# Performance work log

Measured on AMD Instinct MI355X. Metric: run time of the kernel, lower is better.

Reference implementation:

```python
import jax, jax.numpy as jnp
import numpy as np

N, E, G, D, L = 100000, 1600000, 64, 128, 4
CLS_HID, NUM_CLASSES = 256, 10
BN_EPS = 1e-5


def setup_inputs() -> dict:
    key = jax.random.key(0)
    ks = jax.random.split(key, 16)
    s = 0.05
    cls_in = D + L * D  # sum(dims) = 640
    return {
        "node_deg": jax.random.randint(ks[0], (N,), 0, D),
        "edge_index": jax.random.randint(ks[1], (2, E), 0, N),
        "batch_vec": jnp.sort(jax.random.randint(ks[2], (N,), 0, G)),
        "eps": jnp.zeros((L,), jnp.float32),  # GINConv train_eps init 0
        "W1": jax.random.normal(ks[3], (L, D, D), jnp.float32) * s,
        "b1": jax.random.normal(ks[4], (L, D), jnp.float32) * s,
        "W2": jax.random.normal(ks[5], (L, D, D), jnp.float32) * s,
        "b2": jax.random.normal(ks[6], (L, D), jnp.float32) * s,
        "bn_g": jnp.ones((L, D), jnp.float32),
        "bn_b": jnp.zeros((L, D), jnp.float32),
        "Wc1": jax.random.normal(ks[7], (cls_in, CLS_HID), jnp.float32) * s,
        "bc1": jax.random.normal(ks[8], (CLS_HID,), jnp.float32) * s,
        "Wc2": jax.random.normal(ks[9], (CLS_HID, NUM_CLASSES), jnp.float32) * s,
        "bc2": jax.random.normal(ks[10], (NUM_CLASSES,), jnp.float32) * s,
    }


def reference(node_deg, edge_index, batch_vec, eps, W1, b1, W2, b2, bn_g, bn_b, Wc1, bc1, Wc2, bc2):
    n = node_deg.shape[0]
    src, dst = edge_index[0], edge_index[1]
    # OneHotEmbedding of node degree -> initial node features [N, D]
    x = jax.nn.one_hot(node_deg, D, dtype=jnp.float32)
    zs = [x]
    for l in range(eps.shape[0]):
        h_in = zs[-1]
        # GINConv: (1+eps)*x + scatter-add of neighbor features
        agg = jax.ops.segment_sum(h_in[src], dst, num_segments=n)
        h = (1.0 + eps[l]) * h_in + agg
        # mlp: lin -> lrelu -> lin
        h = jax.nn.leaky_relu(h @ W1[l] + b1[l])
        h = h @ W2[l] + b2[l]
        # BatchNorm1d over nodes (training-mode batch stats, biased var)
        mean = h.mean(axis=0)
        var = h.var(axis=0)
        h = (h - mean) * jax.lax.rsqrt(var + BN_EPS) * bn_g[l] + bn_b[l]
        zs.append(jax.nn.leaky_relu(h))
    z = jnp.concatenate(zs, axis=1)  # [N, 640]
    pooled = jax.ops.segment_sum(z, batch_vec, num_segments=G)  # global_add_pool
    pooled = jax.nn.leaky_relu(pooled)
    # classifier head: Linear -> LeakyReLU -> Linear (drop_out=0)
    h = jax.nn.leaky_relu(pooled @ Wc1 + bc1)
    return h @ Wc2 + bc2
```

## Files before the change

kernel.cpp:

```cpp
#include <hip/hip_runtime.h>
#include <hip/hip_bf16.h>


#define N_NODES   100000
#define N_EDGES   1600000
#define N_GRAPHS  64
#define DIM       128
#define N_LAYERS  4
#define CLS_IN    640
#define CLS_HID   256
#define N_CLASSES 10
#define LRELU_SLOPE 0.01f
#define BN_EPS_F    1e-5f

#define NBUCK    782
#define BUCK_CAP 4096
#define ECAP2    1024

typedef __attribute__((ext_vector_type(8))) short bf16x8;
typedef __attribute__((ext_vector_type(4))) float f32x4;

__device__ __forceinline__ float lrelu(float x) { return x > 0.f ? x : LRELU_SLOPE * x; }

__device__ __forceinline__ ushort bf16r(float x) {
    uint a = __float_as_uint(x);
    return (ushort)((a + 0x7FFFu + ((a >> 16) & 1u)) >> 16);
}
__device__ __forceinline__ uint pack2(float x, float y) {
    uint a = __float_as_uint(x), b = __float_as_uint(y);
    a = (a + 0x7FFFu + ((a >> 16) & 1u)) >> 16;
    b = (b + 0x7FFFu + ((b >> 16) & 1u)) >> 16;
    return a | (b << 16);
}
__device__ __forceinline__ float2 unpack2(uint v) {
    return make_float2(__uint_as_float(v << 16), __uint_as_float(v & 0xFFFF0000u));
}

__global__ void k_convert_w(const float* __restrict__ W1, const float* __restrict__ W2,
                            ushort* __restrict__ W1t, ushort* __restrict__ W2t,
                            uint* __restrict__ cursor, float* __restrict__ statsA,
                            float* __restrict__ pooled) {
    int gid = blockIdx.x * blockDim.x + threadIdx.x;
    if (blockIdx.x == 0) {
        for (int i = threadIdx.x; i < NBUCK; i += 256) cursor[i] = 0u;
        for (int i = threadIdx.x; i < 4 * 2 * DIM; i += 256) statsA[i] = 0.f;
    }
    for (int i = gid; i < N_GRAPHS * CLS_IN; i += 512 * 256) pooled[i] = 0.f;
    if (gid >= 8 * DIM * DIM) return;
    int mat = gid >> 14, idx = gid & 16383;
    int k = idx >> 7, n = idx & 127;
    const float* src = (mat < 4) ? (W1 + mat * DIM * DIM) : (W2 + (mat - 4) * DIM * DIM);
    ushort* dst = (mat < 4) ? (W1t + mat * DIM * DIM) : (W2t + (mat - 4) * DIM * DIM);
    dst[n * DIM + k] = bf16r(src[k * DIM + n]);
}

__global__ void k_build_x(const int* __restrict__ deg, const int* __restrict__ batch,
                          uint* __restrict__ x, float* __restrict__ pooled) {
    int gid = blockIdx.x * blockDim.x + threadIdx.x;
    if (gid >= N_NODES * 64) return;
    int i = gid >> 6, c = gid & 63;
    int d = deg[i];
    uint v = 0;
    if ((d >> 1) == c) v = 0x3F80u << (16 * (d & 1));
    x[gid] = v;
    if (c == 0) atomicAdd(&pooled[batch[i] * CLS_IN + d], 1.0f);
}

__global__ void __launch_bounds__(1024) k_partition(const int* __restrict__ src,
                                                    const int* __restrict__ dst,
                                                    uint* __restrict__ cursor,
                                                    uint* __restrict__ ebuf) {
    __shared__ uint hist[NBUCK];
    __shared__ uint basev[NBUCK];
    int t = threadIdx.x;
    for (int b = t; b < NBUCK; b += 1024) hist[b] = 0;
    __syncthreads();
    int e0 = blockIdx.x * 16384;
    uint msrc[16], mdst[16], mrank[16];
#pragma unroll
    for (int i = 0; i < 16; ++i) {
        int e = e0 + i * 1024 + t;
        if (e < N_EDGES) {
            msrc[i] = (uint)src[e];
            mdst[i] = (uint)dst[e];
            mrank[i] = atomicAdd(&hist[mdst[i] >> 7], 1u);
        } else mdst[i] = 0xFFFFFFFFu;
    }
    __syncthreads();
    for (int b = t; b < NBUCK; b += 1024) {
        uint c = hist[b];
        basev[b] = c ? (uint)(b * BUCK_CAP) + atomicAdd(&cursor[b], c) : 0u;
    }
    __syncthreads();
#pragma unroll
    for (int i = 0; i < 16; ++i) {
        if (mdst[i] != 0xFFFFFFFFu) {
            uint b = mdst[i] >> 7;
            ebuf[basev[b] + mrank[i]] = ((mdst[i] & 127u) << 17) | msrc[i];
        }
    }
}

__global__ void __launch_bounds__(1024) k_bases(const uint* __restrict__ cursor,
                                                uint* __restrict__ base,
                                                int* __restrict__ indptr) {
    __shared__ uint sh[1024];
    int t = threadIdx.x;
    uint v = (t < NBUCK) ? min(cursor[t], (uint)BUCK_CAP) : 0u;
    sh[t] = v; __syncthreads();
    for (int off = 1; off < 1024; off <<= 1) {
        uint add = (t >= off) ? sh[t - off] : 0u;
        __syncthreads();
        sh[t] += add;
        __syncthreads();
    }
    if (t < NBUCK) base[t] = sh[t] - v;
    if (t == NBUCK - 1) indptr[N_NODES] = (int)sh[t];
}

__global__ void __launch_bounds__(512) k_sort(const uint* __restrict__ ebuf,
                                              const uint* __restrict__ cursor,
                                              const uint* __restrict__ base,
                                              int* __restrict__ csr,
                                              int* __restrict__ indptr) {
    __shared__ uint sortedL[BUCK_CAP];
    __shared__ uint hist[128];
    __shared__ uint startv[129];
    const int t = threadIdx.x, b = blockIdx.x;
    int cnt = (int)cursor[b]; if (cnt > BUCK_CAP) cnt = BUCK_CAP;
    if (t < 128) hist[t] = 0;
    __syncthreads();
    uint ent[8], rank[8];
    const uint* ep = ebuf + b * BUCK_CAP;
#pragma unroll
    for (int k = 0; k < 8; ++k) {
        int i = t + k * 512;
        if (i < cnt) { ent[k] = ep[i]; rank[k] = atomicAdd(&hist[ent[k] >> 17], 1u); }
    }
    __syncthreads();
    if (t < 128) startv[t + 1] = hist[t];
    if (t == 0) startv[0] = 0;
    __syncthreads();
    for (int off = 1; off < 128; off <<= 1) {
        uint add = (t < 128 && t >= off) ? startv[t + 1 - off] : 0u;
        __syncthreads();
        if (t < 128 && t >= off) startv[t + 1] += add;
        __syncthreads();
    }
#pragma unroll
    for (int k = 0; k < 8; ++k) {
        int i = t + k * 512;
        if (i < cnt) sortedL[startv[ent[k] >> 17] + rank[k]] = ent[k];
    }
    __syncthreads();
    int gbase = (int)base[b];
    for (int i = t; i < cnt; i += 512)
        csr[gbase + i] = (int)(sortedL[i] & 0x1FFFFu);
    if (t < 128) {
        int node = b * 128 + t;
        if (node < N_NODES) indptr[node] = gbase + (int)startv[t];
    }
}

__global__ void __launch_bounds__(128) k_agg6(const uint* __restrict__ h,
                                              const int* __restrict__ indptr,
                                              const int* __restrict__ csr,
                                              uint* __restrict__ out,
                                              const float* __restrict__ epsv, int layer) {
    __shared__ int eL[ECAP2];
    __shared__ int sv[33];
    const int t = threadIdx.x, lane = t & 63, wave = t >> 6;
    const int half = lane >> 5, c = lane & 31;
    const int node0 = blockIdx.x * 32;
    if (t < 33) {
        int n = node0 + t;
        sv[t] = indptr[n > N_NODES ? N_NODES : n];
    }
    __syncthreads();
    const int gbase = sv[0];
    const int cnt = sv[32] - gbase;
    const bool inLds = (cnt <= ECAP2);
    {
        int stg = inLds ? cnt : 0;
        for (int i = t; i < stg; i += 128) eL[i] = csr[gbase + i];
    }
    __syncthreads();
    const float s = 1.0f + epsv[layer];
    for (int ri = 0; ri < 16; ++ri) {
        int r = wave * 16 + ri;
        int g = node0 + r;
        if (g >= N_NODES) break;
        int beg = sv[r] - gbase, end = sv[r + 1] - gbase;
        float a0, a1, a2, a3;
        {
            uint2 own = half ? make_uint2(0u, 0u)
                             : ((const uint2*)(h + (size_t)g * 64))[c];
            float2 o0 = unpack2(own.x), o1 = unpack2(own.y);
            a0 = s * o0.x; a1 = s * o0.y; a2 = s * o1.x; a3 = s * o1.y;
        }
        int j = beg;
        if (inLds) {
            for (; j + 8 <= end; j += 8) {
                int i0 = eL[j + half],     i1 = eL[j + 2 + half];
                int i2 = eL[j + 4 + half], i3 = eL[j + 6 + half];
                uint2 w0 = ((const uint2*)(h + (size_t)i0 * 64))[c];
                uint2 w1 = ((const uint2*)(h + (size_t)i1 * 64))[c];
                uint2 w2 = ((const uint2*)(h + (size_t)i2 * 64))[c];
                uint2 w3 = ((const uint2*)(h + (size_t)i3 * 64))[c];
                float2 p;
                p = unpack2(w0.x); a0 += p.x; a1 += p.y;
                p = unpack2(w0.y); a2 += p.x; a3 += p.y;
                p = unpack2(w1.x); a0 += p.x; a1 += p.y;
                p = unpack2(w1.y); a2 += p.x; a3 += p.y;
                p = unpack2(w2.x); a0 += p.x; a1 += p.y;
                p = unpack2(w2.y); a2 += p.x; a3 += p.y;
                p = unpack2(w3.x); a0 += p.x; a1 += p.y;
                p = unpack2(w3.y); a2 += p.x; a3 += p.y;
            }
            for (; j < end; j += 2) {
                int jj = j + half;
                bool valid = jj < end;
                int iu = eL[valid ? jj : j];
                uint2 w = ((const uint2*)(h + (size_t)iu * 64))[c];
                if (valid) {
                    float2 p;
                    p = unpack2(w.x); a0 += p.x; a1 += p.y;
                    p = unpack2(w.y); a2 += p.x; a3 += p.y;
                }
            }
        } else {
            for (; j < end; j += 2) {
                int jj = j + half;
                bool valid = jj < end;
                int iu = csr[gbase + (valid ? jj : j)];
                uint2 w = ((const uint2*)(h + (size_t)iu * 64))[c];
                if (valid) {
                    float2 p;
                    p = unpack2(w.x); a0 += p.x; a1 += p.y;
                    p = unpack2(w.y); a2 += p.x; a3 += p.y;
                }
            }
        }
        a0 += __shfl_xor(a0, 32);
        a1 += __shfl_xor(a1, 32);
        a2 += __shfl_xor(a2, 32);
        a3 += __shfl_xor(a3, 32);
        if (!half) {
            uint2 o;
            o.x = pack2(a0, a1);
            o.y = pack2(a2, a3);
            ((uint2*)(out + (size_t)g * 64))[c] = o;
        }
    }
}

#define MLP_LDS_BYTES 69632
__global__ void __launch_bounds__(256) k_mlp(const ushort* __restrict__ A,
                                             const ushort* __restrict__ W1t,
                                             const float* __restrict__ b1,
                                             const ushort* __restrict__ W2t,
                                             const float* __restrict__ b2,
                                             ushort* __restrict__ C,
                                             float* __restrict__ stats) {
    __shared__ char pool[MLP_LDS_BYTES];
    ushort* As = (ushort*)pool;
    ushort* Ws = (ushort*)(pool + 34816);
    float*  Cs = (float*)pool;
    const int t = threadIdx.x;
    const int row0 = blockIdx.x * 128;
    {
        int r = t >> 1, hh = t & 1;
        uint4* l = (uint4*)(As + r * 136 + hh * 64);
        if (row0 + r < N_NODES) {
            const uint4* g = (const uint4*)(A + (size_t)(row0 + r) * DIM + hh * 64);
#pragma unroll
            for (int k = 0; k < 8; ++k) l[k] = g[k];
        } else {
            uint4 z = make_uint4(0, 0, 0, 0);
#pragma unroll
            for (int k = 0; k < 8; ++k) l[k] = z;
        }
        const uint4* gw = (const uint4*)(W1t + r * DIM + hh * 64);
        uint4* lw = (uint4*)(Ws + r * 136 + hh * 64);
#pragma unroll
        for (int k = 0; k < 8; ++k) lw[k] = gw[k];
    }
    __syncthreads();
    const int lane = t & 63, wave = t >> 6;
    const int q = lane >> 4, m = lane & 15;
    const int R = (wave >> 1) * 64, Cb = (wave & 1) * 64;
    {
        f32x4 acc[4][4] = {};
#pragma unroll
        for (int ks = 0; ks < 4; ++ks) {
            bf16x8 a[4], b[4];
#pragma unroll
            for (int i = 0; i < 4; ++i)
                a[i] = *(const bf16x8*)(As + (R + i * 16 + m) * 136 + ks * 32 + q * 8);
#pragma unroll
            for (int j = 0; j < 4; ++j)
                b[j] = *(const bf16x8*)(Ws + (Cb + j * 16 + m) * 136 + ks * 32 + q * 8);
#pragma unroll
            for (int i = 0; i < 4; ++i)
#pragma unroll
                for (int j = 0; j < 4; ++j)
                    acc[i][j] = __builtin_amdgcn_mfma_f32_16x16x32_bf16(a[i], b[j], acc[i][j], 0, 0, 0);
        }
        __syncthreads();
        float bias1[4];
#pragma unroll
        for (int j = 0; j < 4; ++j) bias1[j] = b1[Cb + j * 16 + m];
#pragma unroll
        for (int i = 0; i < 4; ++i)
#pragma unroll
            for (int j = 0; j < 4; ++j)
#pragma unroll
                for (int r = 0; r < 4; ++r)
                    As[(R + i * 16 + q * 4 + r) * 136 + Cb + j * 16 + m] =
                        bf16r(lrelu(acc[i][j][r] + bias1[j]));
        {
            int r = t >> 1, hh = t & 1;
            const uint4* gw = (const uint4*)(W2t + r * DIM + hh * 64);
            uint4* lw = (uint4*)(Ws + r * 136 + hh * 64);
#pragma unroll
            for (int k = 0; k < 8; ++k) lw[k] = gw[k];
        }
    }
    __syncthreads();
    f32x4 acc2[4][4] = {};
#pragma unroll
    for (int ks = 0; ks < 4; ++ks) {
        bf16x8 a[4], b[4];
#pragma unroll
        for (int i = 0; i < 4; ++i)
            a[i] = *(const bf16x8*)(As + (R + i * 16 + m) * 136 + ks * 32 + q * 8);
#pragma unroll
        for (int j = 0; j < 4; ++j)
            b[j] = *(const bf16x8*)(Ws + (Cb + j * 16 + m) * 136 + ks * 32 + q * 8);
#pragma unroll
        for (int i = 0; i < 4; ++i)
#pragma unroll
            for (int j = 0; j < 4; ++j)
                acc2[i][j] = __builtin_amdgcn_mfma_f32_16x16x32_bf16(a[i], b[j], acc2[i][j], 0, 0, 0);
    }
    __syncthreads();
    float bias2[4];
#pragma unroll
    for (int j = 0; j < 4; ++j) bias2[j] = b2[Cb + j * 16 + m];
#pragma unroll
    for (int i = 0; i < 4; ++i)
#pragma unroll
        for (int j = 0; j < 4; ++j)
#pragma unroll
            for (int r = 0; r < 4; ++r)
                Cs[(R + i * 16 + q * 4 + r) * 132 + Cb + j * 16 + m] = acc2[i][j][r] + bias2[j];
    __syncthreads();
    if (t < DIM) {
        int rows = N_NODES - row0; if (rows > 128) rows = 128;
        float s1 = 0.f, s2 = 0.f;
        for (int r = 0; r < rows; ++r) { float v = Cs[r * 132 + t]; s1 += v; s2 += v * v; }
        atomicAdd(&stats[t], s1);
        atomicAdd(&stats[DIM + t], s2);
    }
    {
        int r = t >> 1, hh = t & 1;
        if (row0 + r < N_NODES) {
            uint4* outp = (uint4*)(C + (size_t)(row0 + r) * DIM + hh * 64);
#pragma unroll
            for (int k = 0; k < 8; ++k) {
                float4 v0 = *(const float4*)(Cs + r * 132 + hh * 64 + k * 8);
                float4 v1 = *(const float4*)(Cs + r * 132 + hh * 64 + k * 8 + 4);
                uint4 o;
                o.x = pack2(v0.x, v0.y); o.y = pack2(v0.z, v0.w);
                o.z = pack2(v1.x, v1.y); o.w = pack2(v1.z, v1.w);
                outp[k] = o;
            }
        }
    }
}

#define PROWS 64
__global__ void __launch_bounds__(256) k_bnpool(const uint* __restrict__ src,
                                                uint* __restrict__ dst,
                                                const float* __restrict__ stats,
                                                const float* __restrict__ bn_g,
                                                const float* __restrict__ bn_b, int layer,
                                                const int* __restrict__ batch,
                                                float* __restrict__ pooled, int colOff) {
    int c = threadIdx.x & 63;
    int chunk = threadIdx.x >> 6;
    int r0 = blockIdx.x * PROWS + chunk * (PROWS / 4);
    float sc0, sh0, sc1, sh1;
    {
        int f0 = 2 * c, f1 = 2 * c + 1;
        float m0 = stats[f0] * (1.0f / N_NODES);
        float m1 = stats[f1] * (1.0f / N_NODES);
        float v0 = stats[DIM + f0] * (1.0f / N_NODES) - m0 * m0;
        float v1 = stats[DIM + f1] * (1.0f / N_NODES) - m1 * m1;
        sc0 = bn_g[layer * DIM + f0] * rsqrtf(v0 + BN_EPS_F);
        sc1 = bn_g[layer * DIM + f1] * rsqrtf(v1 + BN_EPS_F);
        sh0 = bn_b[layer * DIM + f0] - m0 * sc0;
        sh1 = bn_b[layer * DIM + f1] - m1 * sc1;
    }
    int curg = -1;
    float a0 = 0.f, a1 = 0.f;
    for (int i = 0; i < PROWS / 4; ++i) {
        int r = r0 + i;
        if (r >= N_NODES) break;
        float2 v = unpack2(src[r * 64 + c]);
        float x0 = lrelu(v.x * sc0 + sh0);
        float x1 = lrelu(v.y * sc1 + sh1);
        dst[r * 64 + c] = pack2(x0, x1);
        int g = batch[r];
        if (g != curg) {
            if (curg >= 0) {
                atomicAdd(&pooled[curg * CLS_IN + colOff + 2 * c], a0);
                atomicAdd(&pooled[curg * CLS_IN + colOff + 2 * c + 1], a1);
            }
            curg = g; a0 = 0.f; a1 = 0.f;
        }
        a0 += x0; a1 += x1;
    }
    if (curg >= 0) {
        atomicAdd(&pooled[curg * CLS_IN + colOff + 2 * c], a0);
        atomicAdd(&pooled[curg * CLS_IN + colOff + 2 * c + 1], a1);
    }
}

__global__ void __launch_bounds__(256) k_classifier(const float* __restrict__ pooled,
                                                    const float* __restrict__ Wc1,
                                                    const float* __restrict__ bc1,
                                                    const float* __restrict__ Wc2,
                                                    const float* __restrict__ bc2,
                                                    float* __restrict__ out) {
    __shared__ float p[CLS_IN];
    __shared__ float hh[CLS_HID];
    int g = blockIdx.x, t = threadIdx.x;
    for (int j = t; j < CLS_IN; j += 256) p[j] = lrelu(pooled[g * CLS_IN + j]);
    __syncthreads();
    float acc = bc1[t];
    for (int k = 0; k < CLS_IN; ++k) acc += p[k] * Wc1[k * CLS_HID + t];
    hh[t] = lrelu(acc);
    __syncthreads();
    if (t < N_CLASSES) {
        float a2 = bc2[t];
        for (int k = 0; k < CLS_HID; ++k) a2 += hh[k] * Wc2[k * N_CLASSES + t];
        out[g * N_CLASSES + t] = a2;
    }
}

extern "C" void kernel_launch(void* const* d_in, const int* in_sizes, int n_in,
                              void* d_out, int out_size, void* d_ws, size_t ws_size,
                              hipStream_t stream) {
    const int*   deg   = (const int*)d_in[0];
    const int*   edges = (const int*)d_in[1];
    const int*   srcv  = edges;
    const int*   dstv  = edges + N_EDGES;
    const int*   batch = (const int*)d_in[2];
    const float* epsv  = (const float*)d_in[3];
    const float* W1    = (const float*)d_in[4];
    const float* b1    = (const float*)d_in[5];
    const float* W2    = (const float*)d_in[6];
    const float* b2    = (const float*)d_in[7];
    const float* bn_g  = (const float*)d_in[8];
    const float* bn_b  = (const float*)d_in[9];
    const float* Wc1   = (const float*)d_in[10];
    const float* bc1   = (const float*)d_in[11];
    const float* Wc2   = (const float*)d_in[12];
    const float* bc2   = (const float*)d_in[13];

    char* ws = (char*)d_ws;
    const size_t BUFB = (size_t)N_NODES * DIM * 2;
    size_t off = 0;
    ushort* buf0   = (ushort*)(ws + off); off += BUFB;
    ushort* buf1   = (ushort*)(ws + off); off += BUFB;
    ushort* W1t    = (ushort*)(ws + off); off += 4 * DIM * DIM * 2;
    ushort* W2t    = (ushort*)(ws + off); off += 4 * DIM * DIM * 2;
    float*  pooled = (float*)(ws + off);  off += N_GRAPHS * CLS_IN * 4;
    float*  statsA = (float*)(ws + off);  off += 4 * 2 * DIM * 4;
    uint*   cursor = (uint*)(ws + off);   off += (NBUCK + 8) * 4;
    uint*   base   = (uint*)(ws + off);   off += (NBUCK + 8) * 4;
    int*    indptr = (int*)(ws + off);    off += (N_NODES + 8) * 4;
    int*    csr    = (int*)(ws + off);    off += (size_t)N_EDGES * 4;
    uint*   ebuf   = (uint*)(ws + off);   off += (size_t)NBUCK * BUCK_CAP * 4;

    k_convert_w<<<512, 256, 0, stream>>>(W1, W2, W1t, W2t, cursor, statsA, pooled);
    k_build_x<<<(N_NODES * 64 + 255) / 256, 256, 0, stream>>>(deg, batch, (uint*)buf0, pooled);
    k_partition<<<(N_EDGES + 16383) / 16384, 1024, 0, stream>>>(srcv, dstv, cursor, ebuf);
    k_bases<<<1, 1024, 0, stream>>>(cursor, base, indptr);
    k_sort<<<NBUCK, 512, 0, stream>>>(ebuf, cursor, base, csr, indptr);

    const int gemm_grid = (N_NODES + 127) / 128;
    const int agg_grid  = (N_NODES + 31) / 32;
    for (int l = 0; l < N_LAYERS; ++l) {
        float* stats = statsA + l * 2 * DIM;
        k_agg6<<<agg_grid, 128, 0, stream>>>((const uint*)buf0, indptr, csr,
                                             (uint*)buf1, epsv, l);
        k_mlp<<<gemm_grid, 256, 0, stream>>>(buf1, W1t + l * DIM * DIM, b1 + l * DIM,
                                             W2t + l * DIM * DIM, b2 + l * DIM,
                                             buf1, stats);
        k_bnpool<<<(N_NODES + PROWS - 1) / PROWS, 256, 0, stream>>>(
            (const uint*)buf1, (uint*)buf0, stats, bn_g, bn_b, l, batch,
            pooled, DIM * (l + 1));
    }

    k_classifier<<<N_GRAPHS, 256, 0, stream>>>(pooled, Wc1, bc1, Wc2, bc2, (float*)d_out);
}
```

Measured before the change: 670.3 us.

## Fuse BatchNorm, LeakyReLU and pooling into the next layer's aggregation

The separate per-layer BN/LeakyReLU/pool pass is removed. The MLP now writes raw pre-BN features, and the next layer's aggregation kernel applies the previous layer's BN scale/shift and LeakyReLU on the fly to both the node's own features and every gathered neighbour. The own-node normalized values are also pooled into the graph sums inside that kernel. Only the last layer keeps a standalone pooling kernel. This is meant to save three full read/write passes over the node features, at the cost of redoing the normalization per gathered edge inside the gather loop.

```diff
diff --git a/kernel.cpp b/kernel.cpp
--- a/kernel.cpp
+++ b/kernel.cpp
@@ -20,7 +20,7 @@
 typedef __attribute__((ext_vector_type(8))) short bf16x8;
 typedef __attribute__((ext_vector_type(4))) float f32x4;
 
-__device__ __forceinline__ float lrelu(float x) { return x > 0.f ? x : LRELU_SLOPE * x; }
+__device__ __forceinline__ float lrelu(float x) { return fmaxf(x, LRELU_SLOPE * x); }
 
 __device__ __forceinline__ ushort bf16r(float x) {
     uint a = __float_as_uint(x);
@@ -162,11 +162,16 @@
     }
 }
 
-__global__ void __launch_bounds__(128) k_agg6(const uint* __restrict__ h,
+__global__ void __launch_bounds__(128) k_agg7(const uint* __restrict__ h,
                                               const int* __restrict__ indptr,
                                               const int* __restrict__ csr,
                                               uint* __restrict__ out,
-                                              const float* __restrict__ epsv, int layer) {
+                                              const float* __restrict__ epsv, int layer,
+                                              const float* __restrict__ stats,
+                                              const float* __restrict__ gamma,
+                                              const float* __restrict__ beta,
+                                              const int* __restrict__ batch,
+                                              float* __restrict__ pooled, int colOff) {
     __shared__ int eL[ECAP2];
     __shared__ int sv[33];
     const int t = threadIdx.x, lane = t & 63, wave = t >> 6;
@@ -176,6 +181,21 @@
         int n = node0 + t;
         sv[t] = indptr[n > N_NODES ? N_NODES : n];
     }
+    float sc0 = 1.f, sc1 = 1.f, sc2 = 1.f, sc3 = 1.f;
+    float sh0 = 0.f, sh1 = 0.f, sh2 = 0.f, sh3 = 0.f;
+    const bool doPool = (stats != nullptr);
+    if (doPool) {
+        int f = 4 * c;
+        float m, var, g;
+        m = stats[f] * (1.0f / N_NODES); var = stats[DIM + f] * (1.0f / N_NODES) - m * m;
+        g = gamma[f] * rsqrtf(var + BN_EPS_F); sc0 = g; sh0 = beta[f] - m * g;
+        m = stats[f+1] * (1.0f / N_NODES); var = stats[DIM + f+1] * (1.0f / N_NODES) - m * m;
+        g = gamma[f+1] * rsqrtf(var + BN_EPS_F); sc1 = g; sh1 = beta[f+1] - m * g;
+        m = stats[f+2] * (1.0f / N_NODES); var = stats[DIM + f+2] * (1.0f / N_NODES) - m * m;
+        g = gamma[f+2] * rsqrtf(var + BN_EPS_F); sc2 = g; sh2 = beta[f+2] - m * g;
+        m = stats[f+3] * (1.0f / N_NODES); var = stats[DIM + f+3] * (1.0f / N_NODES) - m * m;
+        g = gamma[f+3] * rsqrtf(var + BN_EPS_F); sc3 = g; sh3 = beta[f+3] - m * g;
+    }
     __syncthreads();
     const int gbase = sv[0];
     const int cnt = sv[32] - gbase;
@@ -186,17 +206,34 @@
     }
     __syncthreads();
     const float s = 1.0f + epsv[layer];
+    int curg = -1;
+    float p0 = 0.f, p1 = 0.f, p2 = 0.f, p3 = 0.f;
     for (int ri = 0; ri < 16; ++ri) {
         int r = wave * 16 + ri;
         int g = node0 + r;
         if (g >= N_NODES) break;
         int beg = sv[r] - gbase, end = sv[r + 1] - gbase;
-        float a0, a1, a2, a3;
-        {
-            uint2 own = half ? make_uint2(0u, 0u)
-                             : ((const uint2*)(h + (size_t)g * 64))[c];
+        float a0 = 0.f, a1 = 0.f, a2 = 0.f, a3 = 0.f;
+        if (!half) {
+            uint2 own = ((const uint2*)(h + (size_t)g * 64))[c];
             float2 o0 = unpack2(own.x), o1 = unpack2(own.y);
-            a0 = s * o0.x; a1 = s * o0.y; a2 = s * o1.x; a3 = s * o1.y;
+            float b0 = lrelu(fmaf(o0.x, sc0, sh0));
+            float b1 = lrelu(fmaf(o0.y, sc1, sh1));
+            float b2 = lrelu(fmaf(o1.x, sc2, sh2));
+            float b3 = lrelu(fmaf(o1.y, sc3, sh3));
+            if (doPool) {
+                int bg = batch[g];
+                if (bg != curg) {
+                    if (curg >= 0) {
+                        float* pp = &pooled[curg * CLS_IN + colOff + 4 * c];
+                        atomicAdd(pp, p0); atomicAdd(pp + 1, p1);
+                        atomicAdd(pp + 2, p2); atomicAdd(pp + 3, p3);
+                    }
+                    curg = bg; p0 = p1 = p2 = p3 = 0.f;
+                }
+                p0 += b0; p1 += b1; p2 += b2; p3 += b3;
+            }
+            a0 = s * b0; a1 = s * b1; a2 = s * b2; a3 = s * b3;
         }
         int j = beg;
         if (inLds) {
@@ -208,14 +245,14 @@
                 uint2 w2 = ((const uint2*)(h + (size_t)i2 * 64))[c];
                 uint2 w3 = ((const uint2*)(h + (size_t)i3 * 64))[c];
                 float2 p;
-                p = unpack2(w0.x); a0 += p.x; a1 += p.y;
-                p = unpack2(w0.y); a2 += p.x; a3 += p.y;
-                p = unpack2(w1.x); a0 += p.x; a1 += p.y;
-                p = unpack2(w1.y); a2 += p.x; a3 += p.y;
-                p = unpack2(w2.x); a0 += p.x; a1 += p.y;
-                p = unpack2(w2.y); a2 += p.x; a3 += p.y;
-                p = unpack2(w3.x); a0 += p.x; a1 += p.y;
-                p = unpack2(w3.y); a2 += p.x; a3 += p.y;
+                p = unpack2(w0.x); a0 += lrelu(fmaf(p.x, sc0, sh0)); a1 += lrelu(fmaf(p.y, sc1, sh1));
+                p = unpack2(w0.y); a2 += lrelu(fmaf(p.x, sc2, sh2)); a3 += lrelu(fmaf(p.y, sc3, sh3));
+                p = unpack2(w1.x); a0 += lrelu(fmaf(p.x, sc0, sh0)); a1 += lrelu(fmaf(p.y, sc1, sh1));
+                p = unpack2(w1.y); a2 += lrelu(fmaf(p.x, sc2, sh2)); a3 += lrelu(fmaf(p.y, sc3, sh3));
+                p = unpack2(w2.x); a0 += lrelu(fmaf(p.x, sc0, sh0)); a1 += lrelu(fmaf(p.y, sc1, sh1));
+                p = unpack2(w2.y); a2 += lrelu(fmaf(p.x, sc2, sh2)); a3 += lrelu(fmaf(p.y, sc3, sh3));
+                p = unpack2(w3.x); a0 += lrelu(fmaf(p.x, sc0, sh0)); a1 += lrelu(fmaf(p.y, sc1, sh1));
+                p = unpack2(w3.y); a2 += lrelu(fmaf(p.x, sc2, sh2)); a3 += lrelu(fmaf(p.y, sc3, sh3));
             }
             for (; j < end; j += 2) {
                 int jj = j + half;
@@ -224,8 +261,8 @@
                 uint2 w = ((const uint2*)(h + (size_t)iu * 64))[c];
                 if (valid) {
                     float2 p;
-                    p = unpack2(w.x); a0 += p.x; a1 += p.y;
-                    p = unpack2(w.y); a2 += p.x; a3 += p.y;
+                    p = unpack2(w.x); a0 += lrelu(fmaf(p.x, sc0, sh0)); a1 += lrelu(fmaf(p.y, sc1, sh1));
+                    p = unpack2(w.y); a2 += lrelu(fmaf(p.x, sc2, sh2)); a3 += lrelu(fmaf(p.y, sc3, sh3));
                 }
             }
         } else {
@@ -236,8 +273,8 @@
                 uint2 w = ((const uint2*)(h + (size_t)iu * 64))[c];
                 if (valid) {
                     float2 p;
-                    p = unpack2(w.x); a0 += p.x; a1 += p.y;
-                    p = unpack2(w.y); a2 += p.x; a3 += p.y;
+                    p = unpack2(w.x); a0 += lrelu(fmaf(p.x, sc0, sh0)); a1 += lrelu(fmaf(p.y, sc1, sh1));
+                    p = unpack2(w.y); a2 += lrelu(fmaf(p.x, sc2, sh2)); a3 += lrelu(fmaf(p.y, sc3, sh3));
                 }
             }
         }
@@ -251,6 +288,11 @@
             o.y = pack2(a2, a3);
             ((uint2*)(out + (size_t)g * 64))[c] = o;
         }
+    }
+    if (doPool && !half && curg >= 0) {
+        float* pp = &pooled[curg * CLS_IN + colOff + 4 * c];
+        atomicAdd(pp, p0); atomicAdd(pp + 1, p1);
+        atomicAdd(pp + 2, p2); atomicAdd(pp + 3, p3);
     }
 }
 
@@ -380,13 +422,12 @@
 }
 
 #define PROWS 64
-__global__ void __launch_bounds__(256) k_bnpool(const uint* __restrict__ src,
-                                                uint* __restrict__ dst,
-                                                const float* __restrict__ stats,
-                                                const float* __restrict__ bn_g,
-                                                const float* __restrict__ bn_b, int layer,
-                                                const int* __restrict__ batch,
-                                                float* __restrict__ pooled, int colOff) {
+__global__ void __launch_bounds__(256) k_pool(const uint* __restrict__ src,
+                                              const float* __restrict__ stats,
+                                              const float* __restrict__ bn_g,
+                                              const float* __restrict__ bn_b,
+                                              const int* __restrict__ batch,
+                                              float* __restrict__ pooled, int colOff) {
     int c = threadIdx.x & 63;
     int chunk = threadIdx.x >> 6;
     int r0 = blockIdx.x * PROWS + chunk * (PROWS / 4);
@@ -397,10 +438,10 @@
         float m1 = stats[f1] * (1.0f / N_NODES);
         float v0 = stats[DIM + f0] * (1.0f / N_NODES) - m0 * m0;
         float v1 = stats[DIM + f1] * (1.0f / N_NODES) - m1 * m1;
-        sc0 = bn_g[layer * DIM + f0] * rsqrtf(v0 + BN_EPS_F);
-        sc1 = bn_g[layer * DIM + f1] * rsqrtf(v1 + BN_EPS_F);
-        sh0 = bn_b[layer * DIM + f0] - m0 * sc0;
-        sh1 = bn_b[layer * DIM + f1] - m1 * sc1;
+        sc0 = bn_g[f0] * rsqrtf(v0 + BN_EPS_F);
+        sc1 = bn_g[f1] * rsqrtf(v1 + BN_EPS_F);
+        sh0 = bn_b[f0] - m0 * sc0;
+        sh1 = bn_b[f1] - m1 * sc1;
     }
     int curg = -1;
     float a0 = 0.f, a1 = 0.f;
@@ -408,9 +449,8 @@
         int r = r0 + i;
         if (r >= N_NODES) break;
         float2 v = unpack2(src[r * 64 + c]);
-        float x0 = lrelu(v.x * sc0 + sh0);
-        float x1 = lrelu(v.y * sc1 + sh1);
-        dst[r * 64 + c] = pack2(x0, x1);
+        float x0 = lrelu(fmaf(v.x, sc0, sh0));
+        float x1 = lrelu(fmaf(v.y, sc1, sh1));
         int g = batch[r];
         if (g != curg) {
             if (curg >= 0) {
@@ -493,16 +533,19 @@
     const int gemm_grid = (N_NODES + 127) / 128;
     const int agg_grid  = (N_NODES + 31) / 32;
     for (int l = 0; l < N_LAYERS; ++l) {
-        float* stats = statsA + l * 2 * DIM;
-        k_agg6<<<agg_grid, 128, 0, stream>>>((const uint*)buf0, indptr, csr,
-                                             (uint*)buf1, epsv, l);
+        const float* pstats = (l == 0) ? nullptr : (statsA + (l - 1) * 2 * DIM);
+        const float* pg = bn_g + (l > 0 ? (l - 1) : 0) * DIM;
+        const float* pb = bn_b + (l > 0 ? (l - 1) : 0) * DIM;
+        k_agg7<<<agg_grid, 128, 0, stream>>>((const uint*)buf0, indptr, csr,
+                                             (uint*)buf1, epsv, l,
+                                             pstats, pg, pb, batch, pooled, DIM * l);
         k_mlp<<<gemm_grid, 256, 0, stream>>>(buf1, W1t + l * DIM * DIM, b1 + l * DIM,
                                              W2t + l * DIM * DIM, b2 + l * DIM,
-                                             buf1, stats);
-        k_bnpool<<<(N_NODES + PROWS - 1) / PROWS, 256, 0, stream>>>(
-            (const uint*)buf1, (uint*)buf0, stats, bn_g, bn_b, l, batch,
-            pooled, DIM * (l + 1));
-    }
+                                             buf0, statsA + l * 2 * DIM);
+    }
+    k_pool<<<(N_NODES + PROWS - 1) / PROWS, 256, 0, stream>>>(
+        (const uint*)buf0, statsA + 3 * 2 * DIM, bn_g + 3 * DIM, bn_b + 3 * DIM,
+        batch, pooled, DIM * 4);
 
     k_classifier<<<N_GRAPHS, 256, 0, stream>>>(pooled, Wc1, bc1, Wc2, bc2, (float*)d_out);
 }
```

Measured after the change: 672.7 us. No clear change (+0.4%).

## Load MLP operands straight from global and compute BN stats in registers

Applied to the files above, without the earlier changes.

The MLP kernel now reads A and W tiles directly from global memory into MFMA fragments instead of staging them through LDS. This shrinks shared memory to a single bf16 tile and allows a higher occupancy launch bound. BatchNorm column sums are reduced in registers with shuffles rather than by a serial per-column LDS scan, and the output is staged as bf16 instead of fp32. Uncoalesced fragment loads from global, a direct dependence on cache hits for the weights, and possible register pressure under the tighter launch bound are the risks; the leaky ReLU and FMA edits are minor.

```diff
diff --git a/kernel.cpp b/kernel.cpp
--- a/kernel.cpp
+++ b/kernel.cpp
@@ -20,7 +20,7 @@
 typedef __attribute__((ext_vector_type(8))) short bf16x8;
 typedef __attribute__((ext_vector_type(4))) float f32x4;
 
-__device__ __forceinline__ float lrelu(float x) { return x > 0.f ? x : LRELU_SLOPE * x; }
+__device__ __forceinline__ float lrelu(float x) { return fmaxf(x, LRELU_SLOPE * x); }
 
 __device__ __forceinline__ ushort bf16r(float x) {
     uint a = __float_as_uint(x);
@@ -254,59 +254,40 @@
     }
 }
 
-#define MLP_LDS_BYTES 69632
-__global__ void __launch_bounds__(256) k_mlp(const ushort* __restrict__ A,
-                                             const ushort* __restrict__ W1t,
-                                             const float* __restrict__ b1,
-                                             const ushort* __restrict__ W2t,
-                                             const float* __restrict__ b2,
-                                             ushort* __restrict__ C,
-                                             float* __restrict__ stats) {
-    __shared__ char pool[MLP_LDS_BYTES];
-    ushort* As = (ushort*)pool;
-    ushort* Ws = (ushort*)(pool + 34816);
-    float*  Cs = (float*)pool;
-    const int t = threadIdx.x;
-    const int row0 = blockIdx.x * 128;
-    {
-        int r = t >> 1, hh = t & 1;
-        uint4* l = (uint4*)(As + r * 136 + hh * 64);
-        if (row0 + r < N_NODES) {
-            const uint4* g = (const uint4*)(A + (size_t)(row0 + r) * DIM + hh * 64);
-#pragma unroll
-            for (int k = 0; k < 8; ++k) l[k] = g[k];
-        } else {
-            uint4 z = make_uint4(0, 0, 0, 0);
-#pragma unroll
-            for (int k = 0; k < 8; ++k) l[k] = z;
-        }
-        const uint4* gw = (const uint4*)(W1t + r * DIM + hh * 64);
-        uint4* lw = (uint4*)(Ws + r * 136 + hh * 64);
-#pragma unroll
-        for (int k = 0; k < 8; ++k) lw[k] = gw[k];
-    }
-    __syncthreads();
-    const int lane = t & 63, wave = t >> 6;
+__global__ void __launch_bounds__(256, 4) k_mlp(const ushort* __restrict__ A,
+                                                const ushort* __restrict__ W1t,
+                                                const float* __restrict__ b1,
+                                                const ushort* __restrict__ W2t,
+                                                const float* __restrict__ b2,
+                                                ushort* __restrict__ C,
+                                                float* __restrict__ stats) {
+    __shared__ ushort As[128 * 136];
+    const int t = threadIdx.x, lane = t & 63, wave = t >> 6;
     const int q = lane >> 4, m = lane & 15;
     const int R = (wave >> 1) * 64, Cb = (wave & 1) * 64;
+    const int row0 = blockIdx.x * 128;
+    const bf16x8 zero8 = {0, 0, 0, 0, 0, 0, 0, 0};
+    f32x4 acc[4][4] = {};
+#pragma unroll
+    for (int ks = 0; ks < 4; ++ks) {
+        bf16x8 a[4], b[4];
+#pragma unroll
+        for (int i = 0; i < 4; ++i) {
+            int row = row0 + R + i * 16 + m;
+            a[i] = (row < N_NODES)
+                 ? *(const bf16x8*)(A + (size_t)row * DIM + ks * 32 + q * 8)
+                 : zero8;
+        }
+#pragma unroll
+        for (int j = 0; j < 4; ++j)
+            b[j] = *(const bf16x8*)(W1t + (Cb + j * 16 + m) * DIM + ks * 32 + q * 8);
+#pragma unroll
+        for (int i = 0; i < 4; ++i)
+#pragma unroll
+            for (int j = 0; j < 4; ++j)
+                acc[i][j] = __builtin_amdgcn_mfma_f32_16x16x32_bf16(a[i], b[j], acc[i][j], 0, 0, 0);
+    }
     {
-        f32x4 acc[4][4] = {};
-#pragma unroll
-        for (int ks = 0; ks < 4; ++ks) {
-            bf16x8 a[4], b[4];
-#pragma unroll
-            for (int i = 0; i < 4; ++i)
-                a[i] = *(const bf16x8*)(As + (R + i * 16 + m) * 136 + ks * 32 + q * 8);
-#pragma unroll
-            for (int j = 0; j < 4; ++j)
-                b[j] = *(const bf16x8*)(Ws + (Cb + j * 16 + m) * 136 + ks * 32 + q * 8);
-#pragma unroll
-            for (int i = 0; i < 4; ++i)
-#pragma unroll
-                for (int j = 0; j < 4; ++j)
-                    acc[i][j] = __builtin_amdgcn_mfma_f32_16x16x32_bf16(a[i], b[j], acc[i][j], 0, 0, 0);
-        }
-        __syncthreads();
         float bias1[4];
 #pragma unroll
         for (int j = 0; j < 4; ++j) bias1[j] = b1[Cb + j * 16 + m];
@@ -318,13 +299,6 @@
                 for (int r = 0; r < 4; ++r)
                     As[(R + i * 16 + q * 4 + r) * 136 + Cb + j * 16 + m] =
                         bf16r(lrelu(acc[i][j][r] + bias1[j]));
-        {
-            int r = t >> 1, hh = t & 1;
-            const uint4* gw = (const uint4*)(W2t + r * DIM + hh * 64);
-            uint4* lw = (uint4*)(Ws + r * 136 + hh * 64);
-#pragma unroll
-            for (int k = 0; k < 8; ++k) lw[k] = gw[k];
-        }
     }
     __syncthreads();
     f32x4 acc2[4][4] = {};
@@ -336,45 +310,59 @@
             a[i] = *(const bf16x8*)(As + (R + i * 16 + m) * 136 + ks * 32 + q * 8);
 #pragma unroll
         for (int j = 0; j < 4; ++j)
-            b[j] = *(const bf16x8*)(Ws + (Cb + j * 16 + m) * 136 + ks * 32 + q * 8);
+            b[j] = *(const bf16x8*)(W2t + (Cb + j * 16 + m) * DIM + ks * 32 + q * 8);
 #pragma unroll
         for (int i = 0; i < 4; ++i)
 #pragma unroll
             for (int j = 0; j < 4; ++j)
                 acc2[i][j] = __builtin_amdgcn_mfma_f32_16x16x32_bf16(a[i], b[j], acc2[i][j], 0, 0, 0);
     }
-    __syncthreads();
-    float bias2[4];
-#pragma unroll
-    for (int j = 0; j < 4; ++j) bias2[j] = b2[Cb + j * 16 + m];
+    {
+        float bias2[4];
+#pragma unroll
+        for (int j = 0; j < 4; ++j) bias2[j] = b2[Cb + j * 16 + m];
+        float s1[4] = {0.f, 0.f, 0.f, 0.f}, s2[4] = {0.f, 0.f, 0.f, 0.f};
+#pragma unroll
+        for (int i = 0; i < 4; ++i)
+#pragma unroll
+            for (int j = 0; j < 4; ++j)
+#pragma unroll
+                for (int r = 0; r < 4; ++r) {
+                    int row = row0 + R + i * 16 + q * 4 + r;
+                    float v = acc2[i][j][r] + bias2[j];
+                    acc2[i][j][r] = v;
+                    if (row < N_NODES) { s1[j] += v; s2[j] += v * v; }
+                }
+#pragma unroll
+        for (int j = 0; j < 4; ++j) {
+            s1[j] += __shfl_xor(s1[j], 16); s1[j] += __shfl_xor(s1[j], 32);
+            s2[j] += __shfl_xor(s2[j], 16); s2[j] += __shfl_xor(s2[j], 32);
+        }
+        if (q == 0) {
+#pragma unroll
+            for (int j = 0; j < 4; ++j) {
+                int col = Cb + j * 16 + m;
+                atomicAdd(&stats[col], s1[j]);
+                atomicAdd(&stats[DIM + col], s2[j]);
+            }
+        }
+    }
+    __syncthreads();
 #pragma unroll
     for (int i = 0; i < 4; ++i)
 #pragma unroll
         for (int j = 0; j < 4; ++j)
 #pragma unroll
             for (int r = 0; r < 4; ++r)
-                Cs[(R + i * 16 + q * 4 + r) * 132 + Cb + j * 16 + m] = acc2[i][j][r] + bias2[j];
-    __syncthreads();
-    if (t < DIM) {
-        int rows = N_NODES - row0; if (rows > 128) rows = 128;
-        float s1 = 0.f, s2 = 0.f;
-        for (int r = 0; r < rows; ++r) { float v = Cs[r * 132 + t]; s1 += v; s2 += v * v; }
-        atomicAdd(&stats[t], s1);
-        atomicAdd(&stats[DIM + t], s2);
-    }
+                As[(R + i * 16 + q * 4 + r) * 136 + Cb + j * 16 + m] = bf16r(acc2[i][j][r]);
+    __syncthreads();
     {
         int r = t >> 1, hh = t & 1;
         if (row0 + r < N_NODES) {
             uint4* outp = (uint4*)(C + (size_t)(row0 + r) * DIM + hh * 64);
-#pragma unroll
-            for (int k = 0; k < 8; ++k) {
-                float4 v0 = *(const float4*)(Cs + r * 132 + hh * 64 + k * 8);
-                float4 v1 = *(const float4*)(Cs + r * 132 + hh * 64 + k * 8 + 4);
-                uint4 o;
-                o.x = pack2(v0.x, v0.y); o.y = pack2(v0.z, v0.w);
-                o.z = pack2(v1.x, v1.y); o.w = pack2(v1.z, v1.w);
-                outp[k] = o;
-            }
+            const uint4* l = (const uint4*)(As + r * 136 + hh * 64);
+#pragma unroll
+            for (int k = 0; k < 8; ++k) outp[k] = l[k];
         }
     }
 }
@@ -408,8 +396,8 @@
         int r = r0 + i;
         if (r >= N_NODES) break;
         float2 v = unpack2(src[r * 64 + c]);
-        float x0 = lrelu(v.x * sc0 + sh0);
-        float x1 = lrelu(v.y * sc1 + sh1);
+        float x0 = lrelu(fmaf(v.x, sc0, sh0));
+        float x1 = lrelu(fmaf(v.y, sc1, sh1));
         dst[r * 64 + c] = pack2(x0, x1);
         int g = batch[r];
         if (g != curg) {
```

Measured after the change: 794.0 us. 18.5% more time.
